# Kernel tuning notes

Measured on AMD Instinct MI355X. Metric: run time of the kernel, lower is better.

The kernel has to match this reference:

```python
import jax, jax.numpy as jnp
import numpy as np

PH = PW = 8
HEADS = 8
ADIM = 256
DH = ADIM // HEADS
N_KEYS = 3
CK, CV, CQ = 16, 32, 16
KS = 7
K_PDIM = PH * PW * CK   # 1024
V_PDIM = PH * PW * CV   # 2048
Q_PDIM = PH * PW * CQ   # 1024
MB_IN = N_KEYS * CV     # 96
MB_HID = 4 * MB_IN      # 384


def _to_patches(x):
    # b c (h ph) (w pw) -> b (h w) (ph pw c)
    b, c, H, W = x.shape
    h, w = H // PH, W // PW
    x = x.reshape(b, c, h, PH, w, PW).transpose(0, 2, 4, 3, 5, 1)
    return x.reshape(b, h * w, PH * PW * c)


def _layernorm(x, g, b):
    m = x.mean(-1, keepdims=True)
    v = x.var(-1, keepdims=True)
    return (x - m) * jax.lax.rsqrt(v + 1e-5) * g + b


def _embed(x, W1, b1, W2, b2):
    # NonLinearEmbedding: Linear -> GELU -> Linear
    return jax.nn.gelu(x @ W1 + b1) @ W2 + b2


def _to_heads(x):
    # b n (h d) -> b h n d
    b, n, hd = x.shape
    return x.reshape(b, n, HEADS, hd // HEADS).transpose(0, 2, 1, 3)


def _conv(x, w, b, groups, pad):
    y = jax.lax.conv_general_dilated(
        x, w, (1, 1), pad,
        dimension_numbers=('NCHW', 'OIHW', 'NCHW'),
        feature_group_count=groups)
    return y + b[None, :, None, None]


def _mbconv(x, w_exp, b_exp, w_dw, b_dw, w_proj, b_proj):
    # grouped 1x1 expand -> GELU -> depthwise kxk -> GELU -> grouped 1x1 project
    h = jax.nn.gelu(_conv(x, w_exp, b_exp, HEADS, 'VALID'))
    h = jax.nn.gelu(_conv(h, w_dw, b_dw, MB_HID, 'SAME'))
    return _conv(h, w_proj, b_proj, HEADS, 'VALID')


def setup_inputs() -> dict:
    key = jax.random.key(0)
    ks = jax.random.split(key, 24)
    B = 2
    key_sizes = [(256, 256), (192, 320), (128, 128)]
    query_sizes = [(256, 256), (192, 192)]
    s = 0.02
    inp = {}
    for i, (h, w) in enumerate(key_sizes):
        inp[f'keys_{i}'] = jax.random.normal(ks[i], (B, CK, h, w), jnp.float32)
        inp[f'values_{i}'] = jax.random.normal(ks[3 + i], (B, CV, h, w), jnp.float32)
    for i, (h, w) in enumerate(query_sizes):
        inp[f'queries_{i}'] = jax.random.normal(ks[6 + i], (B, CQ, h, w), jnp.float32)
    inp['ln_g'] = jnp.ones((V_PDIM,), jnp.float32)
    inp['ln_b'] = jnp.zeros((V_PDIM,), jnp.float32)
    inp['kW1'] = jax.random.normal(ks[8], (K_PDIM, ADIM), jnp.float32) * s
    inp['kb1'] = jnp.zeros((ADIM,), jnp.float32)
    inp['kW2'] = jax.random.normal(ks[9], (ADIM, ADIM), jnp.float32) * s
    inp['kb2'] = jnp.zeros((ADIM,), jnp.float32)
    inp['qW1'] = jax.random.normal(ks[10], (Q_PDIM, ADIM), jnp.float32) * s
    inp['qb1'] = jnp.zeros((ADIM,), jnp.float32)
    inp['qW2'] = jax.random.normal(ks[11], (ADIM, ADIM), jnp.float32) * s
    inp['qb2'] = jnp.zeros((ADIM,), jnp.float32)
    inp['w_exp'] = jax.random.normal(ks[12], (MB_HID, MB_IN // HEADS, 1, 1), jnp.float32) * s
    inp['b_exp'] = jnp.zeros((MB_HID,), jnp.float32)
    inp['w_dw'] = jax.random.normal(ks[13], (MB_HID, 1, KS, KS), jnp.float32) * s
    inp['b_dw'] = jnp.zeros((MB_HID,), jnp.float32)
    inp['w_proj'] = jax.random.normal(ks[14], (CV, MB_HID // HEADS, 1, 1), jnp.float32) * s
    inp['b_proj'] = jnp.zeros((CV,), jnp.float32)
    return inp


def reference(keys_0, keys_1, keys_2, values_0, values_1, values_2,
              queries_0, queries_1, ln_g, ln_b, kW1, kb1, kW2, kb2,
              qW1, qb1, qW2, qb2, w_exp, b_exp, w_dw, b_dw, w_proj, b_proj):
    keys = [keys_0, keys_1, keys_2]
    values = [values_0, values_1, values_2]
    queries = [queries_0, queries_1]
    # spatial sizes are already multiples of (PH, PW) -> pad_to_next_multiple is identity
    query_sizes = [q.shape[-2:] for q in queries]
    kp = [_to_patches(k) for k in keys]
    vp = [_to_patches(v) for v in values]
    qp = [_to_patches(q) for q in queries]
    nk = [p.shape[1] for p in kp]
    nq = [p.shape[1] for p in qp]
    k_seq = jnp.concatenate(kp, axis=1)               # (b, Nk, K_PDIM)
    v_seq = _layernorm(jnp.concatenate(vp, axis=1), ln_g, ln_b)  # (b, Nk, V_PDIM)
    q_seq = jnp.concatenate(qp, axis=1)               # (b, Nq, Q_PDIM)
    k_emb = _to_heads(_embed(k_seq, kW1, kb1, kW2, kb2))  # (b, h, Nk, DH)
    q_emb = _to_heads(_embed(q_seq, qW1, qb1, qW2, qb2))  # (b, h, Nq, DH)
    v_h = _to_heads(v_seq)                                # (b, h, Nk, dv)
    scale = jnp.asarray(1.0 / np.sqrt(DH), k_emb.dtype)
    attn = jnp.einsum('bhid,bhjd->bhij', q_emb, k_emb) * scale
    attn = jax.nn.softmax(attn, axis=-1)
    offs = np.cumsum([0] + nk)
    # per-source weighted values, stacked along a new source axis k
    weighted = jnp.stack(
        [attn[..., offs[i]:offs[i + 1]] @ v_h[:, :, offs[i]:offs[i + 1]]
         for i in range(N_KEYS)], axis=1)              # (b, k, h, Nq, dv)
    qoffs = np.cumsum([0] + nq)
    outs = []
    c = CV // HEADS
    for i, (qh, qw) in enumerate(query_sizes):
        v = weighted[:, :, :, qoffs[i]:qoffs[i + 1]]   # (b, k, hd, n, d)
        b, k, hd, n, d = v.shape
        h, w = qh // PH, qw // PW
        # b k hd (h w) (ph pw c) -> b (hd k c) (h ph) (w pw)
        v = v.reshape(b, k, hd, h, w, PH, PW, c).transpose(0, 2, 1, 7, 3, 5, 4, 6)
        v = v.reshape(b, hd * k * c, h * PH, w * PW)
        outs.append(_mbconv(v, w_exp, b_exp, w_dw, b_dw, w_proj, b_proj))
    return tuple(outs)
```

## Files before the change

kernel.cpp:

```cpp
#include <hip/hip_runtime.h>
#include <hip/hip_bf16.h>
#include <math.h>

typedef unsigned short bfu;
typedef __attribute__((ext_vector_type(8))) short short8v;
typedef __attribute__((ext_vector_type(4))) float f32x4;
typedef __attribute__((ext_vector_type(2))) float f32x2;
typedef struct __attribute__((packed)) { float x, y; } f2p;

__device__ __forceinline__ float fast_rcp(float d) {
    float r = __builtin_amdgcn_rcpf(d);
    return r * fmaf(-d, r, 2.0f);
}
__device__ __forceinline__ f32x2 fma2(f32x2 a, f32x2 b, f32x2 c) {
    return __builtin_elementwise_fma(a, b, c);
}
__device__ __forceinline__ f32x2 splat2(float w) { return (f32x2){w, w}; }
__device__ __forceinline__ float gelu_f(float x) {
    float x3 = x * x * x;
    float e = __expf(1.5957691f * fmaf(0.044715f, x3, x));
    return x * e * __builtin_amdgcn_rcpf(e + 1.0f);
}
__device__ __forceinline__ f32x2 gelu2(f32x2 x) {
    f32x2 x3 = x * x * x;
    f32x2 z = fma2(splat2(0.044715f), x3, x) * 1.5957691f;
    f32x2 e = {__expf(z.x), __expf(z.y)};
    f32x2 d = e + 1.0f;
    f32x2 r = {__builtin_amdgcn_rcpf(d.x), __builtin_amdgcn_rcpf(d.y)};
    return x * e * r;
}
__device__ __forceinline__ float bf2f(bfu u) {
    union { float f; unsigned int i; } v; v.i = ((unsigned int)u) << 16; return v.f;
}
__device__ __forceinline__ bfu f2bf(float f) {
    union { float f; unsigned int i; } v; v.f = f;
    unsigned int r = v.i + 0x7fff + ((v.i >> 16) & 1);
    return (bfu)(r >> 16);
}
__device__ __forceinline__ float ldin(const void* p, size_t i, bool f32) {
    return f32 ? ((const float*)p)[i] : bf2f(((const bfu*)p)[i]);
}
// ... 51 lines not shown
    __shared__ float red[16];
    bool f32 = flag[0] != 0;
    int bid = blockIdx.x;
    int b = bid / 2240, n = bid - b * 2240;
    const void* src; int nl, wp, H, W;
    if (n < 1024)      { src = v0; nl = n;        wp = 32; H = 256; W = 256; }
    else if (n < 1984) { src = v1; nl = n - 1024; wp = 40; H = 192; W = 320; }
    else               { src = v2; nl = n - 1984; wp = 16; H = 128; W = 128; }
    int tid = threadIdx.x;
    int py = nl / wp, px = nl - py * wp;
    int ybase = py * 8, xbase = px * 8;
    float s1 = 0.f, s2 = 0.f;
    #pragma unroll
    for (int i = 0; i < 8; i++) {
        int j = tid + 256 * i;
        int ph = j >> 8, pw = (j >> 5) & 7, c = j & 31;
        float v = ldin(src, ((size_t)(b * 32 + c) * H + ybase + ph) * W + xbase + pw, f32);
        s1 += v; s2 = fmaf(v, v, s2);
    }
    for (int o = 32; o > 0; o >>= 1) { s1 += __shfl_down(s1, o); s2 += __shfl_down(s2, o); }
    int wid = tid >> 6;
    if ((tid & 63) == 0) { red[wid] = s1; red[8 + wid] = s2; }
    __syncthreads();
    if (tid == 0) {
        float a = red[0] + red[1] + red[2] + red[3];
        float q = red[8] + red[9] + red[10] + red[11];
        float m = a * (1.0f / 2048.0f);
        float var = q * (1.0f / 2048.0f) - m * m;
        m_buf[bid] = m;
        i_buf[bid] = 1.0f / sqrtf(var + 1e-5f);
    }
}

__global__ __launch_bounds__(256) void vstage_kernel(
    const void* __restrict__ v0, const void* __restrict__ v1, const void* __restrict__ v2,
    const void* __restrict__ g, const void* __restrict__ beta,
    const int* __restrict__ flag, bfu* __restrict__ out)
{
    __shared__ float red[16];
    __shared__ float mv[2];
    __shared__ __align__(16) bfu Ls[2048];
    bool f32 = flag[0] != 0;
    int bid = blockIdx.x;
    int b = bid / 2240, n = bid - b * 2240;
    const void* src; int nl, wpn, H, W;
    if (n < 1024)      { src = v0; nl = n;        wpn = 32; H = 256; W = 256; }
    else if (n < 1984) { src = v1; nl = n - 1024; wpn = 40; H = 192; W = 320; }
    else               { src = v2; nl = n - 1984; wpn = 16; H = 128; W = 128; }
    int tid = threadIdx.x;
    int py = nl / wpn, px = nl - py * wpn;
    int p = tid & 63;
    int c0 = tid >> 6;
    int y = py * 8 + (p >> 3), x = px * 8 + (p & 7);
    size_t HW = (size_t)H * W;
    size_t base = ((size_t)(b * 32 + c0) * H + y) * W + x;
    float vals[8];
    float s1 = 0.f, s2 = 0.f;
    #pragma unroll
    for (int i = 0; i < 8; i++) {
        float v = ldin(src, base + (size_t)(i << 2) * HW, f32);
        vals[i] = v; s1 += v; s2 = fmaf(v, v, s2);
    }
    for (int o = 32; o > 0; o >>= 1) { s1 += __shfl_down(s1, o); s2 += __shfl_down(s2, o); }
    int wid = tid >> 6;
    if ((tid & 63) == 0) { red[wid] = s1; red[8 + wid] = s2; }
    __syncthreads();
    if (tid == 0) {
        float a = red[0] + red[1] + red[2] + red[3];
        float q = red[8] + red[9] + red[10] + red[11];
        float m = a * (1.0f / 2048.0f);
        float var = q * (1.0f / 2048.0f) - m * m;
        mv[0] = m; mv[1] = 1.0f / sqrtf(var + 1e-5f);
    }
    __syncthreads();
    float m = mv[0], inv = mv[1];
    int jb = (p >> 3) * 256 + (p & 7) * 32 + c0;
    #pragma unroll
    for (int i = 0; i < 8; i++) {
        int j = jb + (i << 2);
        float o = (vals[i] - m) * inv * ldin(g, j, f32) + ldin(beta, j, f32);
        Ls[j] = f2bf(o);
    }
    __syncthreads();
    short8v* dst = (short8v*)(out + (size_t)bid * 2048);
    dst[tid] = ((const short8v*)Ls)[tid];
}

__global__ __launch_bounds__(256) void vtr_kernel(
    const bfu* __restrict__ vseq, bfu* __restrict__ vT)
{
    __shared__ __align__(16) bfu Ls[17408];
    int bid = blockIdx.x;
    int ch = bid % 35;
    int t = bid / 35;
    int h = t & 7, b = t >> 3;
    int c = threadIdx.x;
    const bfu* srcb = vseq + (((size_t)(b * 2240 + (ch << 6))) << 11) + (h << 8) + c;
    #pragma unroll
    for (int k4 = 0; k4 < 16; k4++) {
        ushort4 v;
        v.x = srcb[(size_t)(k4 * 4 + 0) << 11];
        v.y = srcb[(size_t)(k4 * 4 + 1) << 11];
        v.z = srcb[(size_t)(k4 * 4 + 2) << 11];
        v.w = srcb[(size_t)(k4 * 4 + 3) << 11];
        *(ushort4*)&Ls[c * 68 + k4 * 4] = v;
    }
    __syncthreads();
    short8v* dst = (short8v*)(vT + (size_t)((b * 8 + h) * 35 + ch) * 17408);
    const short8v* s = (const short8v*)Ls;
    #pragma unroll
    for (int r = 0; r < 8; r++) dst[(r << 8) + c] = s[(r << 8) + c];
    if (c < 128) dst[2048 + c] = s[2048 + c];
}

__global__ __launch_bounds__(256) void kstage_kernel(
    const void* __restrict__ k0, const void* __restrict__ k1, const void* __restrict__ k2,
    const void* __restrict__ q0, const void* __restrict__ q1,
    const int* __restrict__ flag, bfu* __restrict__ k_seq, bfu* __restrict__ q_seq)
{
    bool f32 = flag[0] != 0;
    int tid = threadIdx.x;
    int w = tid >> 6, l = tid & 63;
    int row = blockIdx.x * 4 + w;
    const void* src; int b, nl, wpn, H, W; bfu* dst;
    if (row < 4480) {
        b = row / 2240; int n = row - b * 2240;
        if (n < 1024)      { src = k0; nl = n;        wpn = 32; H = 256; W = 256; }
        else if (n < 1984) { src = k1; nl = n - 1024; wpn = 40; H = 192; W = 320; }
        else               { src = k2; nl = n - 1984; wpn = 16; H = 128; W = 128; }
        dst = k_seq + ((size_t)row << 10);
    } else {
        int r2 = row - 4480;
        b = r2 / 1600; int n = r2 - b * 1600;
        if (n < 1024)      { src = q0; nl = n;        wpn = 32; H = 256; W = 256; }
        else               { src = q1; nl = n - 1024; wpn = 24; H = 192; W = 192; }
        dst = q_seq + ((size_t)r2 << 10);
    }
    int py = nl / wpn, px = nl - py * wpn;
    int y = (py << 3) + (l >> 3), x = (px << 3) + (l & 7);
    size_t HW = (size_t)H * W;
    size_t base = ((size_t)(b * 16) * H + y) * W + x;
    bfu vals[16];
    #pragma unroll
    for (int c = 0; c < 16; c++) vals[c] = f2bf(ldin(src, base + c * HW, f32));
    bfu* dp = dst + (l << 4);
    *(ushort4*)(dp + 0)  = *(ushort4*)&vals[0];
    *(ushort4*)(dp + 4)  = *(ushort4*)&vals[4];
    *(ushort4*)(dp + 8)  = *(ushort4*)&vals[8];
    *(ushort4*)(dp + 12) = *(ushort4*)&vals[12];
}

__global__ __launch_bounds__(256) void wstage_kernel(
    const void* __restrict__ kW1, const void* __restrict__ qW1,
    const void* __restrict__ kW2, const void* __restrict__ qW2,
    const void* __restrict__ kb1, const void* __restrict__ qb1,
    const void* __restrict__ kb2, const void* __restrict__ qb2,
    const int* __restrict__ flag, bfu* __restrict__ WT, float* __restrict__ biasf)
{
    __shared__ float Ls[64][65];
    bool f32 = flag[0] != 0;
    int bid = blockIdx.x;
    int tid = threadIdx.x;
    if (bid == 160) {
        biasf[tid]       = ldin(kb1, tid, f32);
        biasf[256 + tid] = ldin(qb1, tid, f32);
        biasf[512 + tid] = ldin(kb2, tid, f32);
        biasf[768 + tid] = ldin(qb2, tid, f32);
        return;
    }
    const void* src; bfu* dst; int K, t;
    if (bid < 64)       { src = kW1; dst = WT;          K = 1024; t = bid; }
    else if (bid < 128) { src = qW1; dst = WT + 262144; K = 1024; t = bid - 64; }
    else if (bid < 144) { src = kW2; dst = WT + 524288; K = 256;  t = bid - 128; }
    else                { src = qW2; dst = WT + 589824; K = 256;  t = bid - 144; }
    int ktiles = K >> 6;
    int tk = t % ktiles, tc = t / ktiles;
    int k0 = tk << 6, c0 = tc << 6;
    int j = tid & 63, i0 = tid >> 6;
    #pragma unroll
    for (int p = 0; p < 16; p++) {
        int i = i0 + (p << 2);
        Ls[j][i] = ldin(src, (size_t)(k0 + i) * 256 + c0 + j, f32);
    }
    __syncthreads();
    #pragma unroll
    for (int p = 0; p < 16; p++) {
        int ci = i0 + (p << 2);
        dst[(size_t)(c0 + ci) * K + k0 + j] = f2bf(Ls[ci][j]);
    }
}

__global__ __launch_bounds__(256) void embed_mfma_kernel(
    const bfu* __restrict__ Ak, const bfu* __restrict__ Aq,
    const bfu* __restrict__ WTk, const bfu* __restrict__ WTq,
    const float* __restrict__ bk, const float* __restrict__ bq,
    bfu* __restrict__ Ck, bfu* __restrict__ Cq,
    int K, int gelu, int tiles0)
{
    int bid = blockIdx.x;
    int c0 = (bid & 3) << 6;
    int rt = bid >> 2;
    const bfu* A; const bfu* WT; const float* bias; bfu* C;
    int row0;
    if (rt < tiles0) { A = Ak; WT = WTk; bias = bk; C = Ck; row0 = rt << 6; }
    else             { A = Aq; WT = WTq; bias = bq; C = Cq; row0 = (rt - tiles0) << 6; }
    int tid = threadIdx.x;
    int w = tid >> 6, l = tid & 63;
    int l15 = l & 15, g = l >> 4;
    f32x4 zero4 = {0.f, 0.f, 0.f, 0.f};
    f32x4 acc[4] = {zero4, zero4, zero4, zero4};
    const bfu* wp = WT + (size_t)(c0 + (w << 4) + l15) * K + (g << 3);
    const bfu* ap = A + (size_t)(row0 + l15) * K + (g << 3);
    int nk = K >> 5;
    for (int kk = 0; kk < nk; kk++) {
        short8v af = ld_frag8(wp + (kk << 5));
        #pragma unroll
        for (int r2 = 0; r2 < 4; r2++) {
            short8v bf = ld_frag8(ap + (size_t)(r2 << 4) * K + (kk << 5));
            acc[r2] = __builtin_amdgcn_mfma_f32_16x16x32_bf16(af, bf, acc[r2], 0, 0, 0);
        }
    }
    int colb = c0 + (w << 4) + (g << 2);
// ... 132 lines not shown
            float ar[4] = {a4.x, a4.y, a4.z, a4.w};
            float br[4] = {p0.x, p0.y, p0.z, p0.w};
            #pragma unroll
            for (int rr = 0; rr < 4; rr++)
                #pragma unroll
                for (int i = 0; i < 4; i++)
                    acc[rr][i] = fmaf(ar[rr], br[i], acc[rr][i]);
        }
        __syncthreads();
    }
    int cg = colBase + (tx << 2);
    float bbr[4];
    #pragma unroll
    for (int i = 0; i < 4; i++) bbr[i] = ldin(bias, cg + i, f32);
    #pragma unroll
    for (int rr = 0; rr < 4; rr++) {
        ushort4 o;
        o.x = f2bf(acc[rr][0] + bbr[0]);
        o.y = f2bf(acc[rr][1] + bbr[1]);
        o.z = f2bf(acc[rr][2] + bbr[2]);
        o.w = f2bf(acc[rr][3] + bbr[3]);
        *(ushort4*)(&C[(size_t)(rowBase + (ty << 2) + rr) * 256 + cg]) = o;
    }
}

__global__ __launch_bounds__(256) void attn_mfma3_kernel(
    const bfu* __restrict__ qe, const bfu* __restrict__ ke,
    const bfu* __restrict__ vT,
    bfu* __restrict__ wbuf, float* __restrict__ lbuf3, int h0, int hs)
{
    __shared__ __align__(16) bfu Vs[17408];
    __shared__ __align__(16) bfu Ps[2176];
    __shared__ float red[4][16];
    int bid = blockIdx.x;
    int qtile = bid % 50;
    int t = bid / 50;
    int src3 = t % 3;
    int t2 = t / 3;
    int hh = t2 % hs, b = t2 / hs;
    int h = h0 + hh;
    int n0 = qtile << 5;
    int lo = (src3 == 0) ? 0 : (src3 == 1 ? 16 : 31);
    int hi = (src3 == 0) ? 16 : (src3 == 1 ? 31 : 35);
    int tid = threadIdx.x;
    int w = tid >> 6, l = tid & 63;
    int l15 = l & 15, g = l >> 4;
    int wqt = w >> 1;
    int wkp = (w & 1) << 1;

    short8v qf = *(const short8v*)(qe + (((size_t)(b * 1600 + n0 + (wqt << 4) + l15)) << 8) + (h << 5) + (g << 3));

    f32x4 zero4 = {0.f, 0.f, 0.f, 0.f};
    f32x4 acc[2][4];
    #pragma unroll
    for (int i = 0; i < 2; i++)
        #pragma unroll
        for (int j = 0; j < 4; j++) acc[i][j] = zero4;
    float rs = 0.f;
    const float scale = 0.17677669529663687f;

    const short8v* vbase = (const short8v*)(vT + (size_t)((b * 8 + h) * 35) * 17408);
    short8v* VsV = (short8v*)Vs;

    for (int ch = lo; ch < hi; ch++) {
        const short8v* src = vbase + (size_t)ch * 2176;
        #pragma unroll
        for (int r = 0; r < 8; r++) VsV[(r << 8) + tid] = src[(r << 8) + tid];
        if (tid < 128) VsV[2048 + tid] = src[2048 + tid];
        #pragma unroll
        for (int j = 0; j < 2; j++) {
            int ktile = wkp + j;
            short8v kf = *(const short8v*)(ke + (((size_t)(b * 2240 + (ch << 6) + (ktile << 4) + l15)) << 8) + (h << 5) + (g << 3));
            f32x4 st = __builtin_amdgcn_mfma_f32_16x16x32_bf16(kf, qf, zero4, 0, 0, 0);
            float p0 = __expf(st[0] * scale);
            float p1 = __expf(st[1] * scale);
            float p2 = __expf(st[2] * scale);
            float p3 = __expf(st[3] * scale);
            rs += (p0 + p1) + (p2 + p3);
            ushort4 pk;
            pk.x = f2bf(p0); pk.y = f2bf(p1); pk.z = f2bf(p2); pk.w = f2bf(p3);
            *(ushort4*)&Ps[((wqt << 4) + l15) * 68 + (ktile << 4) + (g << 2)] = pk;
        }
        __syncthreads();
        #pragma unroll
        for (int kt = 0; kt < 2; kt++) {
            short8v a0 = ld_frag8(&Ps[l15 * 68 + (kt << 5) + (g << 3)]);
            short8v a1 = ld_frag8(&Ps[(16 + l15) * 68 + (kt << 5) + (g << 3)]);
            #pragma unroll
            for (int nt = 0; nt < 4; nt++) {
                int ntg = (w << 2) + nt;
                short8v bf = ld_frag8(&Vs[((ntg << 4) + l15) * 68 + (kt << 5) + (g << 3)]);
                acc[0][nt] = __builtin_amdgcn_mfma_f32_16x16x32_bf16(a0, bf, acc[0][nt], 0, 0, 0);
                acc[1][nt] = __builtin_amdgcn_mfma_f32_16x16x32_bf16(a1, bf, acc[1][nt], 0, 0, 0);
            }
        }
        __syncthreads();
    }
    {
        bfu* wb = wbuf + ((size_t)((b * hs + hh) * 3 + src3) * 1600 + n0) * 256 + (w << 6) + l15;
        #pragma unroll
        for (int q2 = 0; q2 < 2; q2++)
            #pragma unroll
            for (int nt = 0; nt < 4; nt++)
                #pragma unroll
                for (int r = 0; r < 4; r++)
                    wb[(size_t)((q2 << 4) + (g << 2) + r) * 256 + (nt << 4)] = f2bf(acc[q2][nt][r]);
    }
    rs += __shfl_xor(rs, 16);
    rs += __shfl_xor(rs, 32);
    if (l < 16) red[w][l15] = rs;
    __syncthreads();
    if (tid < 32) {
        int q2 = tid >> 4;
        float tot = red[q2 << 1][tid & 15] + red[(q2 << 1) + 1][tid & 15];
        lbuf3[src3 * 25600 + (size_t)(b * 8 + h) * 1600 + n0 + tid] = tot;
    }
}

__global__ __launch_bounds__(256) void attn_kernel(
    const bfu* __restrict__ qe, const bfu* __restrict__ ke,
    const bfu* __restrict__ vseq,
    const void* __restrict__ v0, const void* __restrict__ v1, const void* __restrict__ v2,
    const void* __restrict__ ln_g, const void* __restrict__ ln_b,
    const float* __restrict__ m_buf, const float* __restrict__ i_buf,
    const int* __restrict__ flag,
    bfu* __restrict__ wbuf, float* __restrict__ lbuf, int h0, int hs)
{
    __shared__ float Qs[32][36];
    __shared__ float Ks[32][37];
    __shared__ float Ps2[32][37];
    __shared__ float Vls[32][260];
    __shared__ float gbg[256];
    __shared__ float gbb[256];
    bool f32 = flag[0] != 0;
    int bid = blockIdx.x;
    int qt = bid % 50;
    int t = bid / 50;
    int hh = t % hs;
    int b = t / hs;
// ... 106 lines not shown
                acc[rr][2][0] = fmaf(p, w2.x, acc[rr][2][0]);
                acc[rr][2][1] = fmaf(p, w2.y, acc[rr][2][1]);
                acc[rr][2][2] = fmaf(p, w2.z, acc[rr][2][2]);
                acc[rr][2][3] = fmaf(p, w2.w, acc[rr][2][3]);
                acc[rr][3][0] = fmaf(p, w3.x, acc[rr][3][0]);
                acc[rr][3][1] = fmaf(p, w3.y, acc[rr][3][1]);
                acc[rr][3][2] = fmaf(p, w3.z, acc[rr][3][2]);
                acc[rr][3][3] = fmaf(p, w3.w, acc[rr][3][3]);
            }
        }
        __syncthreads();
        if (ch == 31 || ch == 61 || ch == 69) {
            int src = (ch == 31) ? 0 : (ch == 61 ? 1 : 2);
            bfu* wb = wbuf + (size_t)(((b * hs + hh) * 3 + src) * 1600 + n0 + (ty << 1)) * 256 + (tx << 2);
            #pragma unroll
            for (int rr = 0; rr < 2; rr++) {
                #pragma unroll
                for (int q = 0; q < 4; q++) {
                    ushort4 u;
                    u.x = f2bf(acc[rr][q][0]); u.y = f2bf(acc[rr][q][1]);
                    u.z = f2bf(acc[rr][q][2]); u.w = f2bf(acc[rr][q][3]);
                    *(ushort4*)(wb + (size_t)rr * 256 + (q << 6)) = u;
                    acc[rr][q][0] = acc[rr][q][1] = acc[rr][q][2] = acc[rr][q][3] = 0.f;
                }
            }
        }
    }
    if (tid < 32) lbuf[(size_t)(b * 8 + h) * 1600 + n0 + tid] = lreg;
}

__global__ __launch_bounds__(256) void mbconv_kernel(
    const bfu* __restrict__ wbuf, const float* __restrict__ lbuf3,
    const float* __restrict__ wf, const int* __restrict__ flag,
    void* __restrict__ out, size_t out_off, int H, int W, int n_base,
    int tilesX, int tilesY, int h0, int hs)
{
    __shared__ __align__(16) float h1s[8][528];
    __shared__ float h2s[256][9];
    bool f32o = flag[0] != 0;
    const float* wexp_f  = wf;
    const float* bexp_f  = wf + 4608;
    const float* wdw_f   = wf + 4992;
    const float* bdw_f   = wf + 23808;
    const float* wproj_f = wf + 24192;
    const float* bproj_f = wf + 25728;
    int bid = blockIdx.x;
    int gi = bid % hs;
    int t2b = bid / hs;
    int tilesTot = tilesX * tilesY;
    int b = t2b / tilesTot;
    int rem = t2b - b * tilesTot;
    int tY = rem / tilesX, tX = rem - tY * tilesX;
    int gy0 = tY << 4, gx0 = tX << 4;
    int wp = W >> 3;
    int tid = threadIdx.x;
    int wu = __builtin_amdgcn_readfirstlane(tid >> 6);
    int l = tid & 63;
    int doy = ((l >> 3) & 7) << 1;
    int dox = (l & 7) << 1;
    int g = h0 + gi;

    f32x2 xsr2[12];
    #pragma unroll
    for (int ci = 0; ci < 12; ci++) xsr2[ci] = (f32x2){0.f, 0.f};
    int pa0 = 0, pa1 = 0; bool pv0 = false, pv1 = false;
    bool act = tid < 242;
    if (act) {
        #pragma unroll
        for (int j = 0; j < 2; j++) {
            int p = tid * 2 + j;
            int py = p / 22, px = p - py * 22;
            int y = gy0 - 3 + py, x = gx0 - 3 + px;
            bool valid = (y >= 0) && (y < H) && (x >= 0) && (x < W);
            if (j == 0) { pa0 = py * 24 + px; pv0 = valid; }
            else        { pa1 = py * 24 + px; pv1 = valid; }
            if (valid) {
                int n = n_base + (y >> 3) * wp + (x >> 3);
                int li = (b * 8 + g) * 1600 + n;
                float invl = fast_rcp(lbuf3[li] + lbuf3[25600 + li] + lbuf3[51200 + li]);
                int d = ((y & 7) << 5) + ((x & 7) << 2);
                const bfu* src = wbuf + ((size_t)((b * hs + gi) * 3) * 1600 + n) * 256 + d;
                #pragma unroll
                for (int k = 0; k < 3; k++) {
                    ushort4 u = *(const ushort4*)(src + (size_t)k * 409600);
                    if (j == 0) {
                        xsr2[k * 4 + 0].x = bf2f(u.x) * invl;
                        xsr2[k * 4 + 1].x = bf2f(u.y) * invl;
                        xsr2[k * 4 + 2].x = bf2f(u.z) * invl;
                        xsr2[k * 4 + 3].x = bf2f(u.w) * invl;
                    } else {
                        xsr2[k * 4 + 0].y = bf2f(u.x) * invl;
                        xsr2[k * 4 + 1].y = bf2f(u.y) * invl;
                        xsr2[k * 4 + 2].y = bf2f(u.z) * invl;
                        xsr2[k * 4 + 3].y = bf2f(u.w) * invl;
                    }
                }
            }
        }
    }

    float oacc[4] = {0.f, 0.f, 0.f, 0.f};
    for (int chunk = 0; chunk < 6; chunk++) {
        int hc0 = g * 48 + chunk * 8;
        __syncthreads();
        if (act) {
            #pragma unroll
            for (int c = 0; c < 8; c++) {
                const float* we = &wexp_f[(size_t)(hc0 + c) * 12];
                f32x2 a = splat2(bexp_f[hc0 + c]);
                #pragma unroll
                for (int ci = 0; ci < 12; ci++)
                    a = fma2(splat2(we[ci]), xsr2[ci], a);
                f32x2 gv = gelu2(a);
                h1s[c][pa0] = pv0 ? gv.x : 0.f;
                h1s[c][pa1] = pv1 ? gv.y : 0.f;
            }
        }
        __syncthreads();
        #pragma unroll
        for (int c2 = 0; c2 < 2; c2++) {
            int ch = wu + (c2 << 2);
            const float* wd = &wdw_f[(size_t)(hc0 + ch) * 49];
            float bd = bdw_f[hc0 + ch];
            f32x2 a2v0 = splat2(bd);
            f32x2 a2v1 = splat2(bd);
            #pragma unroll
            for (int r = 0; r < 8; r++) {
                const float* hrow = &h1s[ch][(doy + r) * 24 + dox];
                f32x2 p0 = *(const f32x2*)hrow;
                f32x2 p1 = *(const f32x2*)(hrow + 2);
                f32x2 p2 = *(const f32x2*)(hrow + 4);
                f32x2 p3 = *(const f32x2*)(hrow + 6);
                const f2p* qp = (const f2p*)(hrow + 1);
                f32x2 q0 = {qp[0].x, qp[0].y};
                f32x2 q1 = {qp[1].x, qp[1].y};
                f32x2 q2 = {qp[2].x, qp[2].y};
                f32x2 win[7] = {p0, q0, p1, q1, p2, q2, p3};
                if (r <= 6) {
                    const float* wk = &wd[r * 7];
                    #pragma unroll
                    for (int kx = 0; kx < 7; kx++)
                        a2v0 = fma2(splat2(wk[kx]), win[kx], a2v0);
                }
                if (r >= 1) {
                    const float* wk = &wd[(r - 1) * 7];
                    #pragma unroll
                    for (int kx = 0; kx < 7; kx++)
                        a2v1 = fma2(splat2(wk[kx]), win[kx], a2v1);
                }
            }
            f32x2 g0 = gelu2(a2v0), g1 = gelu2(a2v1);
            h2s[(doy + 0) * 16 + dox + 0][ch] = g0.x;
            h2s[(doy + 0) * 16 + dox + 1][ch] = g0.y;
            h2s[(doy + 1) * 16 + dox + 0][ch] = g1.x;
            h2s[(doy + 1) * 16 + dox + 1][ch] = g1.y;
        }
        __syncthreads();
        #pragma unroll
        for (int c = 0; c < 8; c++) {
            float hv = h2s[tid][c];
            #pragma unroll
            for (int oc = 0; oc < 4; oc++)
                oacc[oc] = fmaf(hv, wproj_f[(size_t)(g * 4 + oc) * 48 + chunk * 8 + c], oacc[oc]);
        }
    }
    int yy = tid >> 4, xx = tid & 15;
    #pragma unroll
    for (int oc = 0; oc < 4; oc++) {
        stout(out, out_off + ((size_t)(b * 32 + g * 4 + oc) * H + gy0 + yy) * W + gx0 + xx,
              oacc[oc] + bproj_f[g * 4 + oc], f32o);
    }
}

extern "C" void kernel_launch(void* const* d_in, const int* in_sizes, int n_in,
                              void* d_out, int out_size, void* d_ws, size_t ws_size,
                              hipStream_t stream)
{
    const void *keys0, *keys1, *keys2, *vals0, *vals1, *vals2;
    keys0 = d_in[0];
    if (in_sizes[1] == 4194304) {
        vals0 = d_in[1]; keys1 = d_in[2]; vals1 = d_in[3]; keys2 = d_in[4]; vals2 = d_in[5];
    } else {
        keys1 = d_in[1]; keys2 = d_in[2]; vals0 = d_in[3]; vals1 = d_in[4]; vals2 = d_in[5];
    }
    const void* qrys0  = d_in[6];
    const void* qrys1  = d_in[7];
    const void* ln_g   = d_in[8];
    const void* ln_b   = d_in[9];
    const void* kW1    = d_in[10];
    const void* kb1    = d_in[11];
    const void* kW2    = d_in[12];
    const void* kb2    = d_in[13];
    const void* qW1    = d_in[14];
    const void* qb1    = d_in[15];
    const void* qW2    = d_in[16];
    const void* qb2    = d_in[17];
    const void* w_exp  = d_in[18];
    const void* b_exp  = d_in[19];
    const void* w_dw   = d_in[20];
    const void* b_dw   = d_in[21];
    const void* w_proj = d_in[22];
    const void* b_proj = d_in[23];

    char* base = (char*)d_ws;
    int*   flag  = (int*)base;
    bfu*   k_emb = (bfu*)(base + 64);
    bfu*   q_emb = (bfu*)(base + 64 + 2293760);
    float* m_buf = (float*)(base + 64 + 4034560);
    float* i_buf = (float*)(base + 64 + 4052480);
    const size_t FIXED0 = 4070464ULL;
    float* w_f   = (float*)(base + FIXED0);
    float* lbuf3 = (float*)(base + FIXED0 + 103040);
    const size_t FIXEDN = FIXED0 + 103040ULL + 307200ULL;
    const size_t VTB    = 19496960ULL;
    const size_t RX     = FIXEDN + VTB;

    const size_t EMB = 20975616ULL;
    const size_t need8 = RX + 39321600ULL;
    const size_t need4 = RX + EMB;

    detect_kernel<<<1, 256, 0, stream>>>(keys0, flag);
    wprep_kernel<<<101, 256, 0, stream>>>(w_exp, b_exp, w_dw, b_dw, w_proj, b_proj, flag, w_f);

    if (ws_size >= need4) {
        int hs = (ws_size >= need8) ? 8 : 4;
        bfu*   vT    = (bfu*)(base + FIXEDN);
        bfu*   v_seq = (bfu*)(base + RX);
        bfu*   k_seq = (bfu*)(base + RX);
        bfu*   q_seq = (bfu*)(base + RX + 9175040);
        bfu*   WTb   = (bfu*)(base + RX + 15728640);
        float* biasf = (float*)(base + RX + 17039360);
        bfu*   k_hid = (bfu*)(base + RX + 17043456);
        bfu*   q_hid = (bfu*)(base + RX + 19337216);
        bfu*   w_buf = (bfu*)(base + RX);

        vstage_kernel<<<4480, 256, 0, stream>>>(vals0, vals1, vals2, ln_g, ln_b, flag, v_seq);
        vtr_kernel<<<560, 256, 0, stream>>>(v_seq, vT);
        kstage_kernel<<<1920, 256, 0, stream>>>(keys0, keys1, keys2, qrys0, qrys1,
                                                flag, k_seq, q_seq);
        wstage_kernel<<<161, 256, 0, stream>>>(kW1, qW1, kW2, qW2, kb1, qb1, kb2, qb2,
                                               flag, WTb, biasf);
        embed_mfma_kernel<<<480, 256, 0, stream>>>(k_seq, q_seq, WTb, WTb + 262144,
                                                   biasf, biasf + 256, k_hid, q_hid,
                                                   1024, 1, 70);
        embed_mfma_kernel<<<480, 256, 0, stream>>>(k_hid, q_hid, WTb + 524288, WTb + 589824,
                                                   biasf + 512, biasf + 768, k_emb, q_emb,
                                                   256, 0, 70);
        for (int h0 = 0; h0 < 8; h0 += hs) {
            attn_mfma3_kernel<<<3 * 2 * hs * 50, 256, 0, stream>>>(
                q_emb, k_emb, vT, w_buf, lbuf3, h0, hs);
            mbconv_kernel<<<2 * 256 * hs, 256, 0, stream>>>(
                w_buf, lbuf3, w_f, flag,
                d_out, 0, 256, 256, 0, 16, 16, h0, hs);
            mbconv_kernel<<<2 * 144 * hs, 256, 0, stream>>>(
                w_buf, lbuf3, w_f, flag,
                d_out, 4194304, 192, 192, 1024, 12, 12, h0, hs);
        }
        return;
    }

    int hs;
    if      (ws_size >= FIXEDN + 8ULL * 4915200ULL) hs = 8;
    else if (ws_size >= FIXEDN + 4ULL * 4915200ULL) hs = 4;
    else if (ws_size >= FIXEDN + 2ULL * 4915200ULL) hs = 2;
    else if (ws_size >= FIXEDN + 1ULL * 4915200ULL) hs = 1;
    else {
        zero_out_kernel<<<(out_size + 255) / 256, 256, 0, stream>>>((bfu*)d_out, out_size);
        return;
    }
    char* rest  = base + FIXEDN;
    bfu*  k_hid = (bfu*)rest;
    bfu*  q_hid = (bfu*)(rest + 2293760);
    bfu*  w_buf = (bfu*)rest;

    zero_out_kernel<<<400, 256, 0, stream>>>((bfu*)(lbuf3 + 25600), 102400);
    ln_stats_kernel<<<4480, 256, 0, stream>>>(vals0, vals1, vals2, flag, m_buf, i_buf);
    embed1_kernel<<<480, 256, 0, stream>>>(keys0, keys1, keys2, qrys0, qrys1,
                                           kW1, kb1, qW1, qb1, flag, k_hid, q_hid);
    embed2_kernel<<<480, 256, 0, stream>>>(k_hid, kW2, kb2, k_emb, 70,
                                           q_hid, qW2, qb2, q_emb, flag);
    for (int h0 = 0; h0 < 8; h0 += hs) {
        attn_kernel<<<2 * hs * 50, 256, 0, stream>>>(
            q_emb, k_emb, nullptr, vals0, vals1, vals2, ln_g, ln_b, m_buf, i_buf, flag,
            w_buf, lbuf3, h0, hs);
        mbconv_kernel<<<2 * 256 * hs, 256, 0, stream>>>(
            w_buf, lbuf3, w_f, flag,
            d_out, 0, 256, 256, 0, 16, 16, h0, hs);
        mbconv_kernel<<<2 * 144 * hs, 256, 0, stream>>>(
            w_buf, lbuf3, w_f, flag,
            d_out, 4194304, 192, 192, 1024, 12, 12, h0, hs);
    }
}
```

Before: 548.3 us.

## Merge staging kernels and both mbconv launches, remap block IDs, vectorize mbconv

Folds the value, key/query, weight and mbconv-weight staging kernels into a single launch with a larger workspace layout, so the staging outputs no longer overlap. The two mbconv launches per head group become one launch that picks the query image from the block index. Block IDs in attention and mbconv are permuted in strides of eight, apparently to spread related work across XCDs. Inside mbconv, LDS reads and writes for the depthwise and projection stages become packed float2 operations, and the h2s row is padded to 10. The goal is fewer launches and less instruction overhead, at the cost of needing more workspace before the fast path is taken.

```diff
diff --git a/kernel.cpp b/kernel.cpp
--- a/kernel.cpp
+++ b/kernel.cpp
@@ -6,7 +6,6 @@
 typedef __attribute__((ext_vector_type(8))) short short8v;
 typedef __attribute__((ext_vector_type(4))) float f32x4;
 typedef __attribute__((ext_vector_type(2))) float f32x2;
-typedef struct __attribute__((packed)) { float x, y; } f2p;
 
 __device__ __forceinline__ float fast_rcp(float d) {
     float r = __builtin_amdgcn_rcpf(d);
@@ -124,58 +123,146 @@
     }
 }
 
-__global__ __launch_bounds__(256) void vstage_kernel(
+__global__ __launch_bounds__(256) void stage_all_kernel(
     const void* __restrict__ v0, const void* __restrict__ v1, const void* __restrict__ v2,
-    const void* __restrict__ g, const void* __restrict__ beta,
-    const int* __restrict__ flag, bfu* __restrict__ out)
+    const void* __restrict__ ln_g, const void* __restrict__ ln_b,
+    const void* __restrict__ k0, const void* __restrict__ k1, const void* __restrict__ k2,
+    const void* __restrict__ q0, const void* __restrict__ q1,
+    const void* __restrict__ kW1, const void* __restrict__ qW1,
+    const void* __restrict__ kW2, const void* __restrict__ qW2,
+    const void* __restrict__ kb1, const void* __restrict__ qb1,
+    const void* __restrict__ kb2, const void* __restrict__ qb2,
+    const void* __restrict__ wexp, const void* __restrict__ bexp,
+    const void* __restrict__ wdw, const void* __restrict__ bdw,
+    const void* __restrict__ wproj, const void* __restrict__ bproj,
+    const int* __restrict__ flag,
+    bfu* __restrict__ v_seq, bfu* __restrict__ k_seq, bfu* __restrict__ q_seq,
+    bfu* __restrict__ WT, float* __restrict__ biasf, float* __restrict__ wf)
 {
     __shared__ float red[16];
     __shared__ float mv[2];
-    __shared__ __align__(16) bfu Ls[2048];
+    __shared__ __align__(16) bfu Lb[2048];
+    __shared__ float Lf[64][65];
     bool f32 = flag[0] != 0;
-    int bid = blockIdx.x;
-    int b = bid / 2240, n = bid - b * 2240;
-    const void* src; int nl, wpn, H, W;
-    if (n < 1024)      { src = v0; nl = n;        wpn = 32; H = 256; W = 256; }
-    else if (n < 1984) { src = v1; nl = n - 1024; wpn = 40; H = 192; W = 320; }
-    else               { src = v2; nl = n - 1984; wpn = 16; H = 128; W = 128; }
+    int gbid = blockIdx.x;
     int tid = threadIdx.x;
-    int py = nl / wpn, px = nl - py * wpn;
-    int p = tid & 63;
-    int c0 = tid >> 6;
-    int y = py * 8 + (p >> 3), x = px * 8 + (p & 7);
-    size_t HW = (size_t)H * W;
-    size_t base = ((size_t)(b * 32 + c0) * H + y) * W + x;
-    float vals[8];
-    float s1 = 0.f, s2 = 0.f;
-    #pragma unroll
-    for (int i = 0; i < 8; i++) {
-        float v = ldin(src, base + (size_t)(i << 2) * HW, f32);
-        vals[i] = v; s1 += v; s2 = fmaf(v, v, s2);
-    }
-    for (int o = 32; o > 0; o >>= 1) { s1 += __shfl_down(s1, o); s2 += __shfl_down(s2, o); }
-    int wid = tid >> 6;
-    if ((tid & 63) == 0) { red[wid] = s1; red[8 + wid] = s2; }
-    __syncthreads();
-    if (tid == 0) {
-        float a = red[0] + red[1] + red[2] + red[3];
-        float q = red[8] + red[9] + red[10] + red[11];
-        float m = a * (1.0f / 2048.0f);
-        float var = q * (1.0f / 2048.0f) - m * m;
-        mv[0] = m; mv[1] = 1.0f / sqrtf(var + 1e-5f);
-    }
-    __syncthreads();
-    float m = mv[0], inv = mv[1];
-    int jb = (p >> 3) * 256 + (p & 7) * 32 + c0;
-    #pragma unroll
-    for (int i = 0; i < 8; i++) {
-        int j = jb + (i << 2);
-        float o = (vals[i] - m) * inv * ldin(g, j, f32) + ldin(beta, j, f32);
-        Ls[j] = f2bf(o);
-    }
-    __syncthreads();
-    short8v* dst = (short8v*)(out + (size_t)bid * 2048);
-    dst[tid] = ((const short8v*)Ls)[tid];
+
+    if (gbid < 4480) {
+        int bid = gbid;
+        int b = bid / 2240, n = bid - b * 2240;
+        const void* src; int nl, wpn, H, W;
+        if (n < 1024)      { src = v0; nl = n;        wpn = 32; H = 256; W = 256; }
+        else if (n < 1984) { src = v1; nl = n - 1024; wpn = 40; H = 192; W = 320; }
+        else               { src = v2; nl = n - 1984; wpn = 16; H = 128; W = 128; }
+        int py = nl / wpn, px = nl - py * wpn;
+        int p = tid & 63;
+        int c0 = tid >> 6;
+        int y = py * 8 + (p >> 3), x = px * 8 + (p & 7);
+        size_t HW = (size_t)H * W;
+        size_t base = ((size_t)(b * 32 + c0) * H + y) * W + x;
+        float vals[8];
+        float s1 = 0.f, s2 = 0.f;
+        #pragma unroll
+        for (int i = 0; i < 8; i++) {
+            float v = ldin(src, base + (size_t)(i << 2) * HW, f32);
+            vals[i] = v; s1 += v; s2 = fmaf(v, v, s2);
+        }
+        for (int o = 32; o > 0; o >>= 1) { s1 += __shfl_down(s1, o); s2 += __shfl_down(s2, o); }
+        int wid = tid >> 6;
+        if ((tid & 63) == 0) { red[wid] = s1; red[8 + wid] = s2; }
+        __syncthreads();
+        if (tid == 0) {
+            float a = red[0] + red[1] + red[2] + red[3];
+            float q = red[8] + red[9] + red[10] + red[11];
+            float m = a * (1.0f / 2048.0f);
+            float var = q * (1.0f / 2048.0f) - m * m;
+            mv[0] = m; mv[1] = 1.0f / sqrtf(var + 1e-5f);
+        }
+        __syncthreads();
+        float m = mv[0], inv = mv[1];
+        int jb = (p >> 3) * 256 + (p & 7) * 32 + c0;
+        #pragma unroll
+        for (int i = 0; i < 8; i++) {
+            int j = jb + (i << 2);
+            float o = (vals[i] - m) * inv * ldin(ln_g, j, f32) + ldin(ln_b, j, f32);
+            Lb[j] = f2bf(o);
+        }
+        __syncthreads();
+        short8v* dst = (short8v*)(v_seq + (size_t)bid * 2048);
+        dst[tid] = ((const short8v*)Lb)[tid];
+        return;
+    }
+    if (gbid < 6400) {
+        int w = tid >> 6, l = tid & 63;
+        int row = (gbid - 4480) * 4 + w;
+        const void* src; int b, nl, wpn, H, W; bfu* dst;
+        if (row < 4480) {
+            b = row / 2240; int n = row - b * 2240;
+            if (n < 1024)      { src = k0; nl = n;        wpn = 32; H = 256; W = 256; }
+            else if (n < 1984) { src = k1; nl = n - 1024; wpn = 40; H = 192; W = 320; }
+            else               { src = k2; nl = n - 1984; wpn = 16; H = 128; W = 128; }
+            dst = k_seq + ((size_t)row << 10);
+        } else {
+            int r2 = row - 4480;
+            b = r2 / 1600; int n = r2 - b * 1600;
+            if (n < 1024)      { src = q0; nl = n;        wpn = 32; H = 256; W = 256; }
+            else               { src = q1; nl = n - 1024; wpn = 24; H = 192; W = 192; }
+            dst = q_seq + ((size_t)r2 << 10);
+        }
+        int py = nl / wpn, px = nl - py * wpn;
+        int y = (py << 3) + (l >> 3), x = (px << 3) + (l & 7);
+        size_t HW = (size_t)H * W;
+        size_t base = ((size_t)(b * 16) * H + y) * W + x;
+        bfu vals[16];
+        #pragma unroll
+        for (int c = 0; c < 16; c++) vals[c] = f2bf(ldin(src, base + c * HW, f32));
+        bfu* dp = dst + (l << 4);
+        *(ushort4*)(dp + 0)  = *(ushort4*)&vals[0];
+        *(ushort4*)(dp + 4)  = *(ushort4*)&vals[4];
+        *(ushort4*)(dp + 8)  = *(ushort4*)&vals[8];
+        *(ushort4*)(dp + 12) = *(ushort4*)&vals[12];
+        return;
+    }
+    if (gbid < 6561) {
+        int bid = gbid - 6400;
+        if (bid == 160) {
+            biasf[tid]       = ldin(kb1, tid, f32);
+            biasf[256 + tid] = ldin(qb1, tid, f32);
+            biasf[512 + tid] = ldin(kb2, tid, f32);
+            biasf[768 + tid] = ldin(qb2, tid, f32);
+            return;
+        }
+        const void* src; bfu* dst; int K, t;
+        if (bid < 64)       { src = kW1; dst = WT;          K = 1024; t = bid; }
+        else if (bid < 128) { src = qW1; dst = WT + 262144; K = 1024; t = bid - 64; }
+        else if (bid < 144) { src = kW2; dst = WT + 524288; K = 256;  t = bid - 128; }
+        else                { src = qW2; dst = WT + 589824; K = 256;  t = bid - 144; }
+        int ktiles = K >> 6;
+        int tk = t % ktiles, tc = t / ktiles;
+        int k0i = tk << 6, c0 = tc << 6;
+        int j = tid & 63, i0 = tid >> 6;
+        #pragma unroll
+        for (int p = 0; p < 16; p++) {
+            int i = i0 + (p << 2);
+            Lf[j][i] = ldin(src, (size_t)(k0i + i) * 256 + c0 + j, f32);
+        }
+        __syncthreads();
+        #pragma unroll
+        for (int p = 0; p < 16; p++) {
+            int ci = i0 + (p << 2);
+            dst[(size_t)(c0 + ci) * K + k0i + j] = f2bf(Lf[ci][j]);
+        }
+        return;
+    }
+    {
+        int i = (gbid - 6561) * 256 + tid;
+        if (i < 4608)       wf[i] = ldin(wexp, i, f32);
+        else if (i < 4992)  wf[i] = ldin(bexp, i - 4608, f32);
+        else if (i < 23808) wf[i] = ldin(wdw, i - 4992, f32);
+        else if (i < 24192) wf[i] = ldin(bdw, i - 23808, f32);
+        else if (i < 25728) wf[i] = ldin(wproj, i - 24192, f32);
+        else if (i < 25760) wf[i] = ldin(bproj, i - 25728, f32);
+    }
 }
 
 __global__ __launch_bounds__(256) void vtr_kernel(
@@ -203,83 +290,6 @@
     #pragma unroll
     for (int r = 0; r < 8; r++) dst[(r << 8) + c] = s[(r << 8) + c];
     if (c < 128) dst[2048 + c] = s[2048 + c];
-}
-
-__global__ __launch_bounds__(256) void kstage_kernel(
-    const void* __restrict__ k0, const void* __restrict__ k1, const void* __restrict__ k2,
-    const void* __restrict__ q0, const void* __restrict__ q1,
-    const int* __restrict__ flag, bfu* __restrict__ k_seq, bfu* __restrict__ q_seq)
-{
-    bool f32 = flag[0] != 0;
-    int tid = threadIdx.x;
-    int w = tid >> 6, l = tid & 63;
-    int row = blockIdx.x * 4 + w;
-    const void* src; int b, nl, wpn, H, W; bfu* dst;
-    if (row < 4480) {
-        b = row / 2240; int n = row - b * 2240;
-        if (n < 1024)      { src = k0; nl = n;        wpn = 32; H = 256; W = 256; }
-        else if (n < 1984) { src = k1; nl = n - 1024; wpn = 40; H = 192; W = 320; }
-        else               { src = k2; nl = n - 1984; wpn = 16; H = 128; W = 128; }
-        dst = k_seq + ((size_t)row << 10);
-    } else {
-        int r2 = row - 4480;
-        b = r2 / 1600; int n = r2 - b * 1600;
-        if (n < 1024)      { src = q0; nl = n;        wpn = 32; H = 256; W = 256; }
-        else               { src = q1; nl = n - 1024; wpn = 24; H = 192; W = 192; }
-        dst = q_seq + ((size_t)r2 << 10);
-    }
-    int py = nl / wpn, px = nl - py * wpn;
-    int y = (py << 3) + (l >> 3), x = (px << 3) + (l & 7);
-    size_t HW = (size_t)H * W;
-    size_t base = ((size_t)(b * 16) * H + y) * W + x;
-    bfu vals[16];
-    #pragma unroll
-    for (int c = 0; c < 16; c++) vals[c] = f2bf(ldin(src, base + c * HW, f32));
-    bfu* dp = dst + (l << 4);
-    *(ushort4*)(dp + 0)  = *(ushort4*)&vals[0];
-    *(ushort4*)(dp + 4)  = *(ushort4*)&vals[4];
-    *(ushort4*)(dp + 8)  = *(ushort4*)&vals[8];
-    *(ushort4*)(dp + 12) = *(ushort4*)&vals[12];
-}
-
-__global__ __launch_bounds__(256) void wstage_kernel(
-    const void* __restrict__ kW1, const void* __restrict__ qW1,
-    const void* __restrict__ kW2, const void* __restrict__ qW2,
-    const void* __restrict__ kb1, const void* __restrict__ qb1,
-    const void* __restrict__ kb2, const void* __restrict__ qb2,
-    const int* __restrict__ flag, bfu* __restrict__ WT, float* __restrict__ biasf)
-{
-    __shared__ float Ls[64][65];
-    bool f32 = flag[0] != 0;
-    int bid = blockIdx.x;
-    int tid = threadIdx.x;
-    if (bid == 160) {
-        biasf[tid]       = ldin(kb1, tid, f32);
-        biasf[256 + tid] = ldin(qb1, tid, f32);
-        biasf[512 + tid] = ldin(kb2, tid, f32);
-        biasf[768 + tid] = ldin(qb2, tid, f32);
-        return;
-    }
-    const void* src; bfu* dst; int K, t;
-    if (bid < 64)       { src = kW1; dst = WT;          K = 1024; t = bid; }
-    else if (bid < 128) { src = qW1; dst = WT + 262144; K = 1024; t = bid - 64; }
-    else if (bid < 144) { src = kW2; dst = WT + 524288; K = 256;  t = bid - 128; }
-    else                { src = qW2; dst = WT + 589824; K = 256;  t = bid - 144; }
-    int ktiles = K >> 6;
-    int tk = t % ktiles, tc = t / ktiles;
-    int k0 = tk << 6, c0 = tc << 6;
-    int j = tid & 63, i0 = tid >> 6;
-    #pragma unroll
-    for (int p = 0; p < 16; p++) {
-        int i = i0 + (p << 2);
-        Ls[j][i] = ldin(src, (size_t)(k0 + i) * 256 + c0 + j, f32);
-    }
-    __syncthreads();
-    #pragma unroll
-    for (int p = 0; p < 16; p++) {
-        int ci = i0 + (p << 2);
-        dst[(size_t)(c0 + ci) * K + k0 + j] = f2bf(Ls[ci][j]);
-    }
 }
 
 __global__ __launch_bounds__(256) void embed_mfma_kernel(
@@ -478,7 +488,9 @@
     __shared__ __align__(16) bfu Vs[17408];
     __shared__ __align__(16) bfu Ps[2176];
     __shared__ float red[4][16];
-    int bid = blockIdx.x;
+    int bid0 = blockIdx.x;
+    int cpx = gridDim.x >> 3;
+    int bid = (bid0 & 7) * cpx + (bid0 >> 3);
     int qtile = bid % 50;
     int t = bid / 50;
     int src3 = t % 3;
@@ -543,14 +555,14 @@
         __syncthreads();
     }
     {
-        bfu* wb = wbuf + ((size_t)((b * hs + hh) * 3 + src3) * 1600 + n0) * 256 + (w << 6) + l15;
+        bfu* wbp = wbuf + ((size_t)((b * hs + hh) * 3 + src3) * 1600 + n0) * 256 + (w << 6) + l15;
         #pragma unroll
         for (int q2 = 0; q2 < 2; q2++)
             #pragma unroll
             for (int nt = 0; nt < 4; nt++)
                 #pragma unroll
                 for (int r = 0; r < 4; r++)
-                    wb[(size_t)((q2 << 4) + (g << 2) + r) * 256 + (nt << 4)] = f2bf(acc[q2][nt][r]);
+                    wbp[(size_t)((q2 << 4) + (g << 2) + r) * 256 + (nt << 4)] = f2bf(acc[q2][nt][r]);
     }
     rs += __shfl_xor(rs, 16);
     rs += __shfl_xor(rs, 32);
@@ -723,11 +735,10 @@
 __global__ __launch_bounds__(256) void mbconv_kernel(
     const bfu* __restrict__ wbuf, const float* __restrict__ lbuf3,
     const float* __restrict__ wf, const int* __restrict__ flag,
-    void* __restrict__ out, size_t out_off, int H, int W, int n_base,
-    int tilesX, int tilesY, int h0, int hs)
+    void* __restrict__ out, int h0, int hs)
 {
     __shared__ __align__(16) float h1s[8][528];
-    __shared__ float h2s[256][9];
+    __shared__ float h2s[256][10];
     bool f32o = flag[0] != 0;
     const float* wexp_f  = wf;
     const float* bexp_f  = wf + 4608;
@@ -735,10 +746,16 @@
     const float* bdw_f   = wf + 23808;
     const float* wproj_f = wf + 24192;
     const float* bproj_f = wf + 25728;
-    int bid = blockIdx.x;
-    int gi = bid % hs;
-    int t2b = bid / hs;
+    int bid0 = blockIdx.x;
+    int cpx = gridDim.x >> 3;
+    int bid = (bid0 & 7) * cpx + (bid0 >> 3);
+    int n1 = 512 * hs;
+    size_t out_off; int H, W, n_base, tilesX, tilesY, s;
+    if (bid < n1) { out_off = 0;       H = 256; W = 256; n_base = 0;    tilesX = 16; tilesY = 16; s = bid; }
+    else          { out_off = 4194304; H = 192; W = 192; n_base = 1024; tilesX = 12; tilesY = 12; s = bid - n1; }
     int tilesTot = tilesX * tilesY;
+    int gi = s / (2 * tilesTot);
+    int t2b = s - gi * 2 * tilesTot;
     int b = t2b / tilesTot;
     int rem = t2b - b * tilesTot;
     int tY = rem / tilesX, tX = rem - tY * tilesX;
@@ -754,7 +771,7 @@
     f32x2 xsr2[12];
     #pragma unroll
     for (int ci = 0; ci < 12; ci++) xsr2[ci] = (f32x2){0.f, 0.f};
-    int pa0 = 0, pa1 = 0; bool pv0 = false, pv1 = false;
+    int pa0 = 0; bool pv0 = false, pv1 = false;
     bool act = tid < 242;
     if (act) {
         #pragma unroll
@@ -764,7 +781,7 @@
             int y = gy0 - 3 + py, x = gx0 - 3 + px;
             bool valid = (y >= 0) && (y < H) && (x >= 0) && (x < W);
             if (j == 0) { pa0 = py * 24 + px; pv0 = valid; }
-            else        { pa1 = py * 24 + px; pv1 = valid; }
+            else        { pv1 = valid; }
             if (valid) {
                 int n = n_base + (y >> 3) * wp + (x >> 3);
                 int li = (b * 8 + g) * 1600 + n;
@@ -790,7 +807,7 @@
         }
     }
 
-    float oacc[4] = {0.f, 0.f, 0.f, 0.f};
+    f32x2 oacc2[4] = {splat2(0.f), splat2(0.f), splat2(0.f), splat2(0.f)};
     for (int chunk = 0; chunk < 6; chunk++) {
         int hc0 = g * 48 + chunk * 8;
         __syncthreads();
@@ -803,8 +820,8 @@
                 for (int ci = 0; ci < 12; ci++)
                     a = fma2(splat2(we[ci]), xsr2[ci], a);
                 f32x2 gv = gelu2(a);
-                h1s[c][pa0] = pv0 ? gv.x : 0.f;
-                h1s[c][pa1] = pv1 ? gv.y : 0.f;
+                f32x2 st = { pv0 ? gv.x : 0.f, pv1 ? gv.y : 0.f };
+                *(f32x2*)&h1s[c][pa0] = st;
             }
         }
         __syncthreads();
@@ -817,15 +834,9 @@
             f32x2 a2v1 = splat2(bd);
             #pragma unroll
             for (int r = 0; r < 8; r++) {
-                const float* hrow = &h1s[ch][(doy + r) * 24 + dox];
-                f32x2 p0 = *(const f32x2*)hrow;
-                f32x2 p1 = *(const f32x2*)(hrow + 2);
-                f32x2 p2 = *(const f32x2*)(hrow + 4);
-                f32x2 p3 = *(const f32x2*)(hrow + 6);
-                const f2p* qp = (const f2p*)(hrow + 1);
-                f32x2 q0 = {qp[0].x, qp[0].y};
-                f32x2 q1 = {qp[1].x, qp[1].y};
-                f32x2 q2 = {qp[2].x, qp[2].y};
+                const f32x2* rp = (const f32x2*)&h1s[ch][(doy + r) * 24 + dox];
+                f32x2 p0 = rp[0], p1 = rp[1], p2 = rp[2], p3 = rp[3];
+                f32x2 q0 = {p0.y, p1.x}, q1 = {p1.y, p2.x}, q2 = {p2.y, p3.x};
                 f32x2 win[7] = {p0, q0, p1, q1, p2, q2, p3};
                 if (r <= 6) {
                     const float* wk = &wd[r * 7];
@@ -847,19 +858,25 @@
             h2s[(doy + 1) * 16 + dox + 1][ch] = g1.y;
         }
         __syncthreads();
-        #pragma unroll
-        for (int c = 0; c < 8; c++) {
-            float hv = h2s[tid][c];
-            #pragma unroll
-            for (int oc = 0; oc < 4; oc++)
-                oacc[oc] = fmaf(hv, wproj_f[(size_t)(g * 4 + oc) * 48 + chunk * 8 + c], oacc[oc]);
+        {
+            const f32x2* hp = (const f32x2*)&h2s[tid][0];
+            f32x2 hv[4] = { hp[0], hp[1], hp[2], hp[3] };
+            #pragma unroll
+            for (int oc = 0; oc < 4; oc++) {
+                const float* wpj = &wproj_f[(size_t)(g * 4 + oc) * 48 + chunk * 8];
+                #pragma unroll
+                for (int cp = 0; cp < 4; cp++) {
+                    f32x2 w2 = { wpj[cp * 2], wpj[cp * 2 + 1] };
+                    oacc2[oc] = fma2(hv[cp], w2, oacc2[oc]);
+                }
+            }
         }
     }
     int yy = tid >> 4, xx = tid & 15;
     #pragma unroll
     for (int oc = 0; oc < 4; oc++) {
-        stout(out, out_off + ((size_t)(b * 32 + g * 4 + oc) * H + gy0 + yy) * W + gx0 + xx,
-              oacc[oc] + bproj_f[g * 4 + oc], f32o);
+        float v = oacc2[oc].x + oacc2[oc].y + bproj_f[g * 4 + oc];
+        stout(out, out_off + ((size_t)(b * 32 + g * 4 + oc) * H + gy0 + yy) * W + gx0 + xx, v, f32o);
     }
 }
 
@@ -906,31 +923,31 @@
     const size_t VTB    = 19496960ULL;
     const size_t RX     = FIXEDN + VTB;
 
-    const size_t EMB = 20975616ULL;
+    const size_t EMB = 35393536ULL;
     const size_t need8 = RX + 39321600ULL;
     const size_t need4 = RX + EMB;
 
     detect_kernel<<<1, 256, 0, stream>>>(keys0, flag);
-    wprep_kernel<<<101, 256, 0, stream>>>(w_exp, b_exp, w_dw, b_dw, w_proj, b_proj, flag, w_f);
 
     if (ws_size >= need4) {
         int hs = (ws_size >= need8) ? 8 : 4;
         bfu*   vT    = (bfu*)(base + FIXEDN);
         bfu*   v_seq = (bfu*)(base + RX);
-        bfu*   k_seq = (bfu*)(base + RX);
-        bfu*   q_seq = (bfu*)(base + RX + 9175040);
-        bfu*   WTb   = (bfu*)(base + RX + 15728640);
-        float* biasf = (float*)(base + RX + 17039360);
-        bfu*   k_hid = (bfu*)(base + RX + 17043456);
-        bfu*   q_hid = (bfu*)(base + RX + 19337216);
+        bfu*   k_seq = (bfu*)(base + RX + 18350080);
+        bfu*   q_seq = (bfu*)(base + RX + 27525120);
+        bfu*   WTb   = (bfu*)(base + RX + 34078720);
+        float* biasf = (float*)(base + RX + 35389440);
+        bfu*   k_hid = (bfu*)(base + RX);
+        bfu*   q_hid = (bfu*)(base + RX + 2293760);
         bfu*   w_buf = (bfu*)(base + RX);
 
-        vstage_kernel<<<4480, 256, 0, stream>>>(vals0, vals1, vals2, ln_g, ln_b, flag, v_seq);
+        stage_all_kernel<<<6662, 256, 0, stream>>>(
+            vals0, vals1, vals2, ln_g, ln_b,
+            keys0, keys1, keys2, qrys0, qrys1,
+            kW1, qW1, kW2, qW2, kb1, qb1, kb2, qb2,
+            w_exp, b_exp, w_dw, b_dw, w_proj, b_proj,
+            flag, v_seq, k_seq, q_seq, WTb, biasf, w_f);
         vtr_kernel<<<560, 256, 0, stream>>>(v_seq, vT);
-        kstage_kernel<<<1920, 256, 0, stream>>>(keys0, keys1, keys2, qrys0, qrys1,
-                                                flag, k_seq, q_seq);
-        wstage_kernel<<<161, 256, 0, stream>>>(kW1, qW1, kW2, qW2, kb1, qb1, kb2, qb2,
-                                               flag, WTb, biasf);
         embed_mfma_kernel<<<480, 256, 0, stream>>>(k_seq, q_seq, WTb, WTb + 262144,
                                                    biasf, biasf + 256, k_hid, q_hid,
                                                    1024, 1, 70);
@@ -940,12 +957,8 @@
         for (int h0 = 0; h0 < 8; h0 += hs) {
             attn_mfma3_kernel<<<3 * 2 * hs * 50, 256, 0, stream>>>(
                 q_emb, k_emb, vT, w_buf, lbuf3, h0, hs);
-            mbconv_kernel<<<2 * 256 * hs, 256, 0, stream>>>(
-                w_buf, lbuf3, w_f, flag,
-                d_out, 0, 256, 256, 0, 16, 16, h0, hs);
-            mbconv_kernel<<<2 * 144 * hs, 256, 0, stream>>>(
-                w_buf, lbuf3, w_f, flag,
-                d_out, 4194304, 192, 192, 1024, 12, 12, h0, hs);
+            mbconv_kernel<<<800 * hs, 256, 0, stream>>>(
+                w_buf, lbuf3, w_f, flag, d_out, h0, hs);
         }
         return;
     }
@@ -964,6 +977,7 @@
     bfu*  q_hid = (bfu*)(rest + 2293760);
     bfu*  w_buf = (bfu*)rest;
 
+    wprep_kernel<<<101, 256, 0, stream>>>(w_exp, b_exp, w_dw, b_dw, w_proj, b_proj, flag, w_f);
     zero_out_kernel<<<400, 256, 0, stream>>>((bfu*)(lbuf3 + 25600), 102400);
     ln_stats_kernel<<<4480, 256, 0, stream>>>(vals0, vals1, vals2, flag, m_buf, i_buf);
     embed1_kernel<<<480, 256, 0, stream>>>(keys0, keys1, keys2, qrys0, qrys1,
@@ -974,11 +988,7 @@
         attn_kernel<<<2 * hs * 50, 256, 0, stream>>>(
             q_emb, k_emb, nullptr, vals0, vals1, vals2, ln_g, ln_b, m_buf, i_buf, flag,
             w_buf, lbuf3, h0, hs);
-        mbconv_kernel<<<2 * 256 * hs, 256, 0, stream>>>(
-            w_buf, lbuf3, w_f, flag,
-            d_out, 0, 256, 256, 0, 16, 16, h0, hs);
-        mbconv_kernel<<<2 * 144 * hs, 256, 0, stream>>>(
-            w_buf, lbuf3, w_f, flag,
-            d_out, 4194304, 192, 192, 1024, 12, 12, h0, hs);
-    }
-}
+        mbconv_kernel<<<800 * hs, 256, 0, stream>>>(
+            w_buf, lbuf3, w_f, flag, d_out, h0, hs);
+    }
+}
```

Result: faster. 526.4 us (-4.0%).
